# Kernel tuning notes

Measured on AMD Instinct MI355X. Metric: run time of the kernel, lower is better.

## Reference

```python
import jax, jax.numpy as jnp
import numpy as np

DIM = 1024
NU = 1
INNER = 2 * DIM * NU  # 2048
BATCH = 32


def dpfp(x, nu=NU):
    # x: [b, d] -> [b, 2*d*nu]
    x = jnp.concatenate([jax.nn.relu(x), jax.nn.relu(-x)], axis=-1)
    x_rolled = jnp.concatenate([jnp.roll(x, j, axis=-1) for j in range(1, nu + 1)], axis=-1)
    x_repeat = jnp.concatenate([x] * nu, axis=-1)
    return x_repeat * x_rolled


def setup_inputs() -> dict:
    key = jax.random.key(0)
    ks = jax.random.split(key, 12)
    s_d = 1.0 / np.sqrt(DIM)
    s_i = 1.0 / np.sqrt(INNER)
    return {
        "x": jax.random.normal(ks[0], (BATCH, DIM), jnp.float32),
        "W": jax.random.normal(ks[1], (BATCH, INNER, INNER), jnp.float32) * 0.02,
        "Wq": jax.random.uniform(ks[2], (DIM, DIM), jnp.float32, -s_d, s_d),
        "bq": jax.random.uniform(ks[3], (DIM,), jnp.float32, -s_d, s_d),
        "Wk": jax.random.uniform(ks[4], (DIM, DIM), jnp.float32, -s_d, s_d),
        "bk": jax.random.uniform(ks[5], (DIM,), jnp.float32, -s_d, s_d),
        "Wv": jax.random.uniform(ks[6], (DIM, INNER), jnp.float32, -s_d, s_d),
        "bv": jax.random.uniform(ks[7], (INNER,), jnp.float32, -s_d, s_d),
        "Wo": jax.random.uniform(ks[8], (INNER, DIM), jnp.float32, -s_i, s_i),
        "bo": jax.random.uniform(ks[9], (DIM,), jnp.float32, -s_i, s_i),
        "Wb": jax.random.uniform(ks[10], (DIM, 1), jnp.float32, -s_d, s_d),
        "bb": jax.random.uniform(ks[11], (1,), jnp.float32, -s_d, s_d),
    }


def reference(x, W, Wq, bq, Wk, bk, Wv, bv, Wo, bo, Wb, bb):
    # context = x (default)
    q = x @ Wq + bq              # [b, dim]
    k = x @ Wk + bk              # [b, dim]
    v = x @ Wv + bv              # [b, inner]
    beta = jax.nn.sigmoid(x @ Wb + bb)  # [b, 1]

    kp = dpfp(k)                 # [b, inner]
    # einsum 'bij,bj->bj': sum over i of W, elementwise-times kp (as written in source)
    vo = W.sum(axis=1) * kp      # [b, inner]
    dv = beta * (v - vo)         # [b, inner]
    W_new = W + dv[:, :, None] * kp[:, None, :]  # [b, inner, inner]

    qp = dpfp(q)                 # [b, inner]
    # einsum 'bij,bi->bi': sum over j of W_new, elementwise-times qp
    outv = W_new.sum(axis=2) * qp  # [b, inner]
    out = outv @ Wo + bo           # [b, dim]
    return (out, W_new)
```

## Files before the change

### kernel.cpp

```cpp
#include <hip/hip_runtime.h>
#include <math.h>

#define DIM    1024
#define INNER  2048
#define BATCH  32
#define NCHUNK 16
#define CROWS  128

__device__ __forceinline__ float4 f4add(float4 a, float4 b) {
    return make_float4(a.x + b.x, a.y + b.y, a.z + b.z, a.w + b.w);
}

__global__ __launch_bounds__(256) void pre_kernel(
    const float* __restrict__ x,
    const float* __restrict__ Wq, const float* __restrict__ bq,
    const float* __restrict__ Wk, const float* __restrict__ bk,
    const float* __restrict__ Wv, const float* __restrict__ bv,
    const float* __restrict__ W,
    float* __restrict__ q, float* __restrict__ k, float* __restrict__ v,
    float* __restrict__ colpart, float* __restrict__ rowsum)
{
    __shared__ float4 sh[4][512];
    const int bid = blockIdx.x;
    const int t   = threadIdx.x;

    if (bid < BATCH * NCHUNK) {
        const int b     = bid & (BATCH - 1);
        const int chunk = bid >> 5;
        const int i0    = chunk * CROWS;
        const int wave  = t >> 6, lane = t & 63;
        const float4* Wp = (const float4*)(W + (size_t)b * INNER * INNER);

        float4 csum[8];
        #pragma unroll
        for (int c = 0; c < 8; ++c) csum[c] = make_float4(0.f, 0.f, 0.f, 0.f);

        for (int r = wave; r < CROWS; r += 4) {
            const size_t rb = (size_t)(i0 + r) * (INNER / 4);
            float4 w4[8];
            #pragma unroll
            for (int c = 0; c < 8; ++c) w4[c] = Wp[rb + lane + 64 * c];
            #pragma unroll
            for (int c = 0; c < 8; ++c) csum[c] = f4add(csum[c], w4[c]);
            float4 racc = f4add(f4add(f4add(w4[0], w4[1]), f4add(w4[2], w4[3])),
                                f4add(f4add(w4[4], w4[5]), f4add(w4[6], w4[7])));
            float s = (racc.x + racc.y) + (racc.z + racc.w);
            #pragma unroll
            for (int m = 1; m < 64; m <<= 1) s += __shfl_xor(s, m, 64);
            if (lane == 0) rowsum[b * INNER + i0 + r] = s;
        }
        #pragma unroll
        for (int c = 0; c < 8; ++c) sh[wave][lane + 64 * c] = csum[c];
        __syncthreads();
        float4* cp = (float4*)colpart + (size_t)(b * NCHUNK + chunk) * (INNER / 4);
        #pragma unroll
        for (int c2 = 0; c2 < 2; ++c2) {
            const int c4 = t + 256 * c2;
            cp[c4] = f4add(f4add(sh[0][c4], sh[1][c4]), f4add(sh[2][c4], sh[3][c4]));
        }
    } else {
        const int idx = bid - BATCH * NCHUNK;
        const int b   = idx & (BATCH - 1);
        float* xs = (float*)sh;
        const float4* xsrc = (const float4*)(x + b * DIM);
        float4* xdst = (float4*)xs;
        for (int i = t; i < DIM / 4; i += 256) xdst[i] = xsrc[i];
        __syncthreads();

        const int c = (idx >> 5) * 256 + t;
        const float* Wm; const float* bias; float* outp; int N, n;
        if (c < DIM)          { Wm = Wq; bias = bq; outp = q; N = DIM;   n = c;           }
        else if (c < 2 * DIM) { Wm = Wk; bias = bk; outp = k; N = DIM;   n = c - DIM;     }
        else                  { Wm = Wv; bias = bv; outp = v; N = INNER; n = c - 2 * DIM; }

        float acc = 0.f;
        #pragma unroll 8
        for (int kk = 0; kk < DIM; ++kk)
            acc += xs[kk] * Wm[(size_t)kk * N + n];
        outp[(size_t)b * N + n] = acc + bias[n];
    }
}

__device__ __forceinline__ float xcf(const float* __restrict__ kb, int j) {
    float val = (j < DIM) ? kb[j] : -kb[j - DIM];
    return fmaxf(val, 0.f);
}

__global__ __launch_bounds__(256) void vec_kernel(
    const float* __restrict__ x, const float* __restrict__ Wb, const float* __restrict__ bb,
    const float* __restrict__ q, const float* __restrict__ k, const float* __restrict__ v,
    const float* __restrict__ colpart, const float* __restrict__ rowsum,
    float* __restrict__ kp, float* __restrict__ dv, float* __restrict__ outv)
{
    __shared__ float kb_s[DIM], qb_s[DIM];
    __shared__ float red1[4], red2[4];
    const int b = blockIdx.x, t = threadIdx.x;
    const int wave = t >> 6, lane = t & 63;

    const float* xrow = x + b * DIM;
    float bsum = 0.f;
    for (int i = t; i < DIM; i += 256) {
        kb_s[i] = k[b * DIM + i];
        qb_s[i] = q[b * DIM + i];
        bsum += xrow[i] * Wb[i];
    }
    #pragma unroll
    for (int m = 1; m < 64; m <<= 1) bsum += __shfl_xor(bsum, m, 64);
    if (lane == 0) red1[wave] = bsum;
    __syncthreads();
    const float beta = 1.f / (1.f + expf(-((red1[0] + red1[1] + red1[2] + red1[3]) + bb[0])));

    float skp = 0.f, dvu[8], ru[8];
    #pragma unroll
    for (int u = 0; u < 8; ++u) {
        const int j = u * 256 + t;
        float cs = 0.f;
        #pragma unroll
        for (int c = 0; c < NCHUNK; ++c)
            cs += colpart[(size_t)(b * NCHUNK + c) * INNER + j];
        const float kpj = xcf(kb_s, j) * xcf(kb_s, (j + INNER - 1) & (INNER - 1));
        kp[b * INNER + j] = kpj;
        skp += kpj;
        const float dvj = beta * (v[b * INNER + j] - cs * kpj);
        dvu[u] = dvj;
        dv[b * INNER + j] = dvj;
        ru[u] = rowsum[b * INNER + j];
    }
    #pragma unroll
    for (int m = 1; m < 64; m <<= 1) skp += __shfl_xor(skp, m, 64);
    if (lane == 0) red2[wave] = skp;
    __syncthreads();
    const float S = red2[0] + red2[1] + red2[2] + red2[3];

    #pragma unroll
    for (int u = 0; u < 8; ++u) {
        const int j = u * 256 + t;
        const float qpj = xcf(qb_s, j) * xcf(qb_s, (j + INNER - 1) & (INNER - 1));
        outv[b * INNER + j] = (ru[u] + dvu[u] * S) * qpj;
    }
}

__global__ __launch_bounds__(256) void post_kernel(
    const float* __restrict__ outv, const float* __restrict__ Wo,
    const float* __restrict__ bo, float* __restrict__ out,
    const float* __restrict__ W, const float* __restrict__ dv,
    const float* __restrict__ kp, float* __restrict__ Wn)
{
    const int bid = blockIdx.x;
    const int t   = threadIdx.x;
    if (bid < 512) {
        __shared__ float os[INNER];
        __shared__ float part[4][64];
        const int b    = bid & (BATCH - 1);
        const int n0   = (bid >> 5) * 64;
        const int wave = t >> 6, lane = t & 63;

        const float4* src = (const float4*)(outv + b * INNER);
        float4* dst = (float4*)os;
        for (int i = t; i < INNER / 4; i += 256) dst[i] = src[i];
        __syncthreads();

        const float* Wcol = Wo + n0 + lane;
        const int ibase = wave * 512;
        float acc = 0.f;
        #pragma unroll 8
        for (int i = 0; i < 512; ++i)
            acc += os[ibase + i] * Wcol[(size_t)(ibase + i) * DIM];
        part[wave][lane] = acc;
        __syncthreads();
        if (t < 64)
            out[b * DIM + n0 + t] =
                ((part[0][t] + part[1][t]) + (part[2][t] + part[3][t])) + bo[n0 + t];
    } else {
        const int wb = bid - 512;
        const int b  = wb >> 11;
        const float d = dv[wb];
        const float4* kp4 = (const float4*)(kp + b * INNER);
        const float4* Wr  = (const float4*)W  + ((size_t)wb << 9);
        float4*       Wnr = (float4*)Wn       + ((size_t)wb << 9);
        float4 w0 = Wr[t],       k0 = kp4[t];
        float4 w1 = Wr[t + 256], k1 = kp4[t + 256];
        w0.x += d * k0.x; w0.y += d * k0.y; w0.z += d * k0.z; w0.w += d * k0.w;
        w1.x += d * k1.x; w1.y += d * k1.y; w1.z += d * k1.z; w1.w += d * k1.w;
        Wnr[t]       = w0;
        Wnr[t + 256] = w1;
    }
}

extern "C" void kernel_launch(void* const* d_in, const int* in_sizes, int n_in,
                              void* d_out, int out_size, void* d_ws, size_t ws_size,
                              hipStream_t stream)
{
    const float* x  = (const float*)d_in[0];
    const float* W  = (const float*)d_in[1];
    const float* Wq = (const float*)d_in[2];
    const float* bq = (const float*)d_in[3];
    const float* Wk = (const float*)d_in[4];
    const float* bk = (const float*)d_in[5];
    const float* Wv = (const float*)d_in[6];
    const float* bv = (const float*)d_in[7];
    const float* Wo = (const float*)d_in[8];
    const float* bo = (const float*)d_in[9];
    const float* Wb = (const float*)d_in[10];
    const float* bb = (const float*)d_in[11];

    float* out = (float*)d_out;
    float* Wn  = (float*)d_out + (size_t)BATCH * DIM;

    float* ws = (float*)d_ws;
    float* q       = ws;
    float* k       = q + BATCH * DIM;
    float* v       = k + BATCH * DIM;
    float* rowsum  = v + BATCH * INNER;
    float* kp      = rowsum + BATCH * INNER;
    float* dv      = kp + BATCH * INNER;
    float* outv    = dv + BATCH * INNER;
    float* colpart = outv + BATCH * INNER;

    pre_kernel<<<dim3(BATCH * NCHUNK + 512), 256, 0, stream>>>(
        x, Wq, bq, Wk, bk, Wv, bv, W, q, k, v, colpart, rowsum);
    vec_kernel<<<dim3(BATCH), 256, 0, stream>>>(
        x, Wb, bb, q, k, v, colpart, rowsum, kp, dv, outv);
    post_kernel<<<dim3(512 + BATCH * INNER), 256, 0, stream>>>(
        outv, Wo, bo, out, W, dv, kp, Wn);
}
```

Baseline: 1.021 ms.

## Rework W reduction and update: more chunks, smem row sums, 4-row update blocks

The W column/row reduction now splits into 32 chunks of 64 rows, loads two rows per iteration, and computes row sums through a shared-memory partial table instead of per-row wave shuffles. The rank-1 update kernel processes four rows per block and walks batches in reverse order, likely to hit W rows still resident in cache from the reduction pass. The vec kernel is vectorized with float4 accesses. This adds a serialized cross-wave accumulation loop and doubles the colpart traffic.

```diff
diff --git a/kernel.cpp b/kernel.cpp
--- a/kernel.cpp
+++ b/kernel.cpp
@@ -4,11 +4,18 @@
 #define DIM    1024
 #define INNER  2048
 #define BATCH  32
-#define NCHUNK 16
-#define CROWS  128
+#define WCHUNK 32
+#define CR     64
 
 __device__ __forceinline__ float4 f4add(float4 a, float4 b) {
     return make_float4(a.x + b.x, a.y + b.y, a.z + b.z, a.w + b.w);
+}
+
+__device__ __forceinline__ float hsum8(const float4* w) {
+    float4 a = f4add(f4add(w[0], w[1]), f4add(w[2], w[3]));
+    float4 b = f4add(f4add(w[4], w[5]), f4add(w[6], w[7]));
+    float4 c = f4add(a, b);
+    return (c.x + c.y) + (c.z + c.w);
 }
 
 __global__ __launch_bounds__(256) void pre_kernel(
@@ -20,14 +27,15 @@
     float* __restrict__ q, float* __restrict__ k, float* __restrict__ v,
     float* __restrict__ colpart, float* __restrict__ rowsum)
 {
-    __shared__ float4 sh[4][512];
+    __shared__ float  rowpart[CR][66];
+    __shared__ float4 csumsh[512];
     const int bid = blockIdx.x;
     const int t   = threadIdx.x;
 
-    if (bid < BATCH * NCHUNK) {
+    if (bid < BATCH * WCHUNK) {
         const int b     = bid & (BATCH - 1);
         const int chunk = bid >> 5;
-        const int i0    = chunk * CROWS;
+        const int i0    = chunk * CR;
         const int wave  = t >> 6, lane = t & 63;
         const float4* Wp = (const float4*)(W + (size_t)b * INNER * INNER);
 
@@ -35,33 +43,51 @@
         #pragma unroll
         for (int c = 0; c < 8; ++c) csum[c] = make_float4(0.f, 0.f, 0.f, 0.f);
 
-        for (int r = wave; r < CROWS; r += 4) {
-            const size_t rb = (size_t)(i0 + r) * (INNER / 4);
-            float4 w4[8];
-            #pragma unroll
-            for (int c = 0; c < 8; ++c) w4[c] = Wp[rb + lane + 64 * c];
-            #pragma unroll
-            for (int c = 0; c < 8; ++c) csum[c] = f4add(csum[c], w4[c]);
-            float4 racc = f4add(f4add(f4add(w4[0], w4[1]), f4add(w4[2], w4[3])),
-                                f4add(f4add(w4[4], w4[5]), f4add(w4[6], w4[7])));
-            float s = (racc.x + racc.y) + (racc.z + racc.w);
-            #pragma unroll
-            for (int m = 1; m < 64; m <<= 1) s += __shfl_xor(s, m, 64);
-            if (lane == 0) rowsum[b * INNER + i0 + r] = s;
-        }
-        #pragma unroll
-        for (int c = 0; c < 8; ++c) sh[wave][lane + 64 * c] = csum[c];
-        __syncthreads();
-        float4* cp = (float4*)colpart + (size_t)(b * NCHUNK + chunk) * (INNER / 4);
-        #pragma unroll
-        for (int c2 = 0; c2 < 2; ++c2) {
-            const int c4 = t + 256 * c2;
-            cp[c4] = f4add(f4add(sh[0][c4], sh[1][c4]), f4add(sh[2][c4], sh[3][c4]));
+        for (int j = 0; j < 16; j += 2) {
+            const int ra = 4 * j + wave;
+            const int rb = ra + 4;
+            const size_t ba = (size_t)(i0 + ra) * (INNER / 4);
+            const size_t bb = (size_t)(i0 + rb) * (INNER / 4);
+            float4 wa[8], wb[8];
+            #pragma unroll
+            for (int c = 0; c < 8; ++c) wa[c] = Wp[ba + lane + 64 * c];
+            #pragma unroll
+            for (int c = 0; c < 8; ++c) wb[c] = Wp[bb + lane + 64 * c];
+            #pragma unroll
+            for (int c = 0; c < 8; ++c)
+                csum[c] = f4add(csum[c], f4add(wa[c], wb[c]));
+            rowpart[ra][lane] = hsum8(wa);
+            rowpart[rb][lane] = hsum8(wb);
+        }
+
+        for (int wv = 0; wv < 4; ++wv) {
+            __syncthreads();
+            if (wave == wv) {
+                #pragma unroll
+                for (int c = 0; c < 8; ++c) {
+                    if (wv == 0) csumsh[lane + 64 * c] = csum[c];
+                    else csumsh[lane + 64 * c] = f4add(csumsh[lane + 64 * c], csum[c]);
+                }
+            }
+        }
+        __syncthreads();
+
+        float4* cp = (float4*)colpart + (size_t)(b * WCHUNK + chunk) * (INNER / 4);
+        cp[t]       = csumsh[t];
+        cp[t + 256] = csumsh[t + 256];
+
+        if (t < 128) {
+            const int r = t >> 1, half = t & 1;
+            float s = 0.f;
+            #pragma unroll
+            for (int l = 0; l < 32; ++l) s += rowpart[r][half * 32 + l];
+            s += __shfl_xor(s, 1, 64);
+            if (half == 0) rowsum[b * INNER + i0 + r] = s;
         }
     } else {
-        const int idx = bid - BATCH * NCHUNK;
+        const int idx = bid - BATCH * WCHUNK;
         const int b   = idx & (BATCH - 1);
-        float* xs = (float*)sh;
+        float* xs = (float*)csumsh;
         const float4* xsrc = (const float4*)(x + b * DIM);
         float4* xdst = (float4*)xs;
         for (int i = t; i < DIM / 4; i += 256) xdst[i] = xsrc[i];
@@ -97,47 +123,66 @@
     const int b = blockIdx.x, t = threadIdx.x;
     const int wave = t >> 6, lane = t & 63;
 
+    ((float4*)kb_s)[t] = ((const float4*)(k + b * DIM))[t];
+    ((float4*)qb_s)[t] = ((const float4*)(q + b * DIM))[t];
     const float* xrow = x + b * DIM;
     float bsum = 0.f;
-    for (int i = t; i < DIM; i += 256) {
-        kb_s[i] = k[b * DIM + i];
-        qb_s[i] = q[b * DIM + i];
-        bsum += xrow[i] * Wb[i];
-    }
+    for (int i = t; i < DIM; i += 256) bsum += xrow[i] * Wb[i];
     #pragma unroll
     for (int m = 1; m < 64; m <<= 1) bsum += __shfl_xor(bsum, m, 64);
     if (lane == 0) red1[wave] = bsum;
     __syncthreads();
     const float beta = 1.f / (1.f + expf(-((red1[0] + red1[1] + red1[2] + red1[3]) + bb[0])));
 
-    float skp = 0.f, dvu[8], ru[8];
+    float4 cs_a = make_float4(0.f, 0.f, 0.f, 0.f);
+    float4 cs_b = make_float4(0.f, 0.f, 0.f, 0.f);
+    #pragma unroll 4
+    for (int c = 0; c < WCHUNK; ++c) {
+        const float4* cp = (const float4*)colpart + (size_t)(b * WCHUNK + c) * (INNER / 4);
+        cs_a = f4add(cs_a, cp[t]);
+        cs_b = f4add(cs_b, cp[t + 256]);
+    }
+
+    const int ja = 4 * t, jb = DIM + 4 * t;
+    float kpa[4], kpb[4], skp = 0.f;
     #pragma unroll
-    for (int u = 0; u < 8; ++u) {
-        const int j = u * 256 + t;
-        float cs = 0.f;
-        #pragma unroll
-        for (int c = 0; c < NCHUNK; ++c)
-            cs += colpart[(size_t)(b * NCHUNK + c) * INNER + j];
-        const float kpj = xcf(kb_s, j) * xcf(kb_s, (j + INNER - 1) & (INNER - 1));
-        kp[b * INNER + j] = kpj;
-        skp += kpj;
-        const float dvj = beta * (v[b * INNER + j] - cs * kpj);
-        dvu[u] = dvj;
-        dv[b * INNER + j] = dvj;
-        ru[u] = rowsum[b * INNER + j];
-    }
+    for (int e = 0; e < 4; ++e) {
+        kpa[e] = xcf(kb_s, ja + e) * xcf(kb_s, (ja + e + INNER - 1) & (INNER - 1));
+        kpb[e] = xcf(kb_s, jb + e) * xcf(kb_s, (jb + e + INNER - 1) & (INNER - 1));
+        skp += kpa[e] + kpb[e];
+    }
+    ((float4*)(kp + b * INNER))[t]       = make_float4(kpa[0], kpa[1], kpa[2], kpa[3]);
+    ((float4*)(kp + b * INNER))[t + 256] = make_float4(kpb[0], kpb[1], kpb[2], kpb[3]);
+
+    const float4 v_a = ((const float4*)(v + b * INNER))[t];
+    const float4 v_b = ((const float4*)(v + b * INNER))[t + 256];
+    float4 dva, dvb;
+    dva.x = beta * (v_a.x - cs_a.x * kpa[0]); dva.y = beta * (v_a.y - cs_a.y * kpa[1]);
+    dva.z = beta * (v_a.z - cs_a.z * kpa[2]); dva.w = beta * (v_a.w - cs_a.w * kpa[3]);
+    dvb.x = beta * (v_b.x - cs_b.x * kpb[0]); dvb.y = beta * (v_b.y - cs_b.y * kpb[1]);
+    dvb.z = beta * (v_b.z - cs_b.z * kpb[2]); dvb.w = beta * (v_b.w - cs_b.w * kpb[3]);
+    ((float4*)(dv + b * INNER))[t]       = dva;
+    ((float4*)(dv + b * INNER))[t + 256] = dvb;
+
     #pragma unroll
     for (int m = 1; m < 64; m <<= 1) skp += __shfl_xor(skp, m, 64);
     if (lane == 0) red2[wave] = skp;
     __syncthreads();
     const float S = red2[0] + red2[1] + red2[2] + red2[3];
 
-    #pragma unroll
-    for (int u = 0; u < 8; ++u) {
-        const int j = u * 256 + t;
-        const float qpj = xcf(qb_s, j) * xcf(qb_s, (j + INNER - 1) & (INNER - 1));
-        outv[b * INNER + j] = (ru[u] + dvu[u] * S) * qpj;
-    }
+    const float4 ru_a = ((const float4*)(rowsum + b * INNER))[t];
+    const float4 ru_b = ((const float4*)(rowsum + b * INNER))[t + 256];
+    float4 oa, ob;
+    oa.x = (ru_a.x + dva.x * S) * (xcf(qb_s, ja + 0) * xcf(qb_s, (ja + 0 + INNER - 1) & (INNER - 1)));
+    oa.y = (ru_a.y + dva.y * S) * (xcf(qb_s, ja + 1) * xcf(qb_s, (ja + 1 + INNER - 1) & (INNER - 1)));
+    oa.z = (ru_a.z + dva.z * S) * (xcf(qb_s, ja + 2) * xcf(qb_s, (ja + 2 + INNER - 1) & (INNER - 1)));
+    oa.w = (ru_a.w + dva.w * S) * (xcf(qb_s, ja + 3) * xcf(qb_s, (ja + 3 + INNER - 1) & (INNER - 1)));
+    ob.x = (ru_b.x + dvb.x * S) * (xcf(qb_s, jb + 0) * xcf(qb_s, (jb + 0 + INNER - 1) & (INNER - 1)));
+    ob.y = (ru_b.y + dvb.y * S) * (xcf(qb_s, jb + 1) * xcf(qb_s, (jb + 1 + INNER - 1) & (INNER - 1)));
+    ob.z = (ru_b.z + dvb.z * S) * (xcf(qb_s, jb + 2) * xcf(qb_s, (jb + 2 + INNER - 1) & (INNER - 1)));
+    ob.w = (ru_b.w + dvb.w * S) * (xcf(qb_s, jb + 3) * xcf(qb_s, (jb + 3 + INNER - 1) & (INNER - 1)));
+    ((float4*)(outv + b * INNER))[t]       = oa;
+    ((float4*)(outv + b * INNER))[t + 256] = ob;
 }
 
 __global__ __launch_bounds__(256) void post_kernel(
@@ -172,18 +217,38 @@
             out[b * DIM + n0 + t] =
                 ((part[0][t] + part[1][t]) + (part[2][t] + part[3][t])) + bo[n0 + t];
     } else {
-        const int wb = bid - 512;
-        const int b  = wb >> 11;
-        const float d = dv[wb];
-        const float4* kp4 = (const float4*)(kp + b * INNER);
-        const float4* Wr  = (const float4*)W  + ((size_t)wb << 9);
-        float4*       Wnr = (float4*)Wn       + ((size_t)wb << 9);
-        float4 w0 = Wr[t],       k0 = kp4[t];
-        float4 w1 = Wr[t + 256], k1 = kp4[t + 256];
-        w0.x += d * k0.x; w0.y += d * k0.y; w0.z += d * k0.z; w0.w += d * k0.w;
-        w1.x += d * k1.x; w1.y += d * k1.y; w1.z += d * k1.z; w1.w += d * k1.w;
-        Wnr[t]       = w0;
-        Wnr[t + 256] = w1;
+        const int idx = bid - 512;
+        const int blk = (BATCH * (INNER / 4) - 1) - idx;
+        const int b   = blk >> 9;
+        const int r0  = (blk & 511) << 2;
+
+        const float4* kp4 = (const float4*)(kp + (size_t)b * INNER);
+        const float4 k0 = kp4[t], k1 = kp4[t + 256];
+
+        const float* dvb = dv + (size_t)b * INNER + r0;
+        float dloc[4];
+        #pragma unroll
+        for (int r = 0; r < 4; ++r) dloc[r] = dvb[r];
+
+        const size_t rowbase = (size_t)(b * INNER + r0) * (INNER / 4);
+        const float4* Wb4 = (const float4*)W + rowbase;
+        float4*       Wn4 = (float4*)Wn + rowbase;
+
+        float4 w[8];
+        #pragma unroll
+        for (int r = 0; r < 4; ++r) {
+            w[2 * r]     = Wb4[(size_t)r * (INNER / 4) + t];
+            w[2 * r + 1] = Wb4[(size_t)r * (INNER / 4) + t + 256];
+        }
+        #pragma unroll
+        for (int r = 0; r < 4; ++r) {
+            const float d = dloc[r];
+            float4 a = w[2 * r], c = w[2 * r + 1];
+            a.x += d * k0.x; a.y += d * k0.y; a.z += d * k0.z; a.w += d * k0.w;
+            c.x += d * k1.x; c.y += d * k1.y; c.z += d * k1.z; c.w += d * k1.w;
+            Wn4[(size_t)r * (INNER / 4) + t]       = a;
+            Wn4[(size_t)r * (INNER / 4) + t + 256] = c;
+        }
     }
 }
 
@@ -217,10 +282,10 @@
     float* outv    = dv + BATCH * INNER;
     float* colpart = outv + BATCH * INNER;
 
-    pre_kernel<<<dim3(BATCH * NCHUNK + 512), 256, 0, stream>>>(
+    pre_kernel<<<dim3(BATCH * WCHUNK + 512), 256, 0, stream>>>(
         x, Wq, bq, Wk, bk, Wv, bv, W, q, k, v, colpart, rowsum);
     vec_kernel<<<dim3(BATCH), 256, 0, stream>>>(
         x, Wb, bb, q, k, v, colpart, rowsum, kp, dv, outv);
-    post_kernel<<<dim3(512 + BATCH * INNER), 256, 0, stream>>>(
+    post_kernel<<<dim3(512 + BATCH * (INNER / 4)), 256, 0, stream>>>(
         outv, Wo, bo, out, W, dv, kp, Wn);
 }
```

New measurement: 1.037 ms. No clear change (+1.6%).
